# Performance work log

Measured on AMD Instinct MI355X. Metric: run time of the kernel, lower is better.

The kernel has to match this reference:

```python
import jax, jax.numpy as jnp
import numpy as np

FEATURE_HEIGHT = 50
FEATURE_WIDTH = 50


def setup_inputs() -> dict:
    key = jax.random.key(0)
    k1, k2, k3 = jax.random.split(key, 3)
    bs, K, H, D = 16, FEATURE_HEIGHT * FEATURE_WIDTH, 8, 32
    Q, L, P = 2000, 1, 4
    value = jax.random.normal(k1, (bs, K, H, D), dtype=jnp.float32)
    value_spatial_shapes = jnp.array([[FEATURE_HEIGHT, FEATURE_WIDTH]], dtype=jnp.int64)
    sampling_locations = jax.random.uniform(k2, (bs, Q, H, L, P, 2), dtype=jnp.float32)
    attention_weights = jax.random.uniform(k3, (bs, Q, H, L, P), dtype=jnp.float32)
    return {
        "value": value,
        "value_spatial_shapes": value_spatial_shapes,
        "sampling_locations": sampling_locations,
        "attention_weights": attention_weights,
    }


def _bilinear_sample(img, grid):
    """torch.F.grid_sample(mode='bilinear', padding_mode='zeros', align_corners=False).

    img:  (N, D, h, w)
    grid: (N, Q, P, 2), last dim (x, y) in [-1, 1]
    returns (N, D, Q, P)
    """
    N, D, h, w = img.shape
    # unnormalize (align_corners=False)
    x = (grid[..., 0] + 1.0) * (w * 0.5) - 0.5  # (N, Q, P)
    y = (grid[..., 1] + 1.0) * (h * 0.5) - 0.5
    x0 = jnp.floor(x)
    y0 = jnp.floor(y)
    x1 = x0 + 1.0
    y1 = y0 + 1.0
    wx1 = x - x0
    wx0 = 1.0 - wx1
    wy1 = y - y0
    wy0 = 1.0 - wy1

    img_flat = img.reshape(N, D, h * w)

    def corner(ix, iy, wgt):
        valid = ((ix >= 0) & (ix < w) & (iy >= 0) & (iy < h)).astype(img.dtype)
        ixc = jnp.clip(ix, 0, w - 1).astype(jnp.int32)
        iyc = jnp.clip(iy, 0, h - 1).astype(jnp.int32)
        idx = (iyc * w + ixc).reshape(N, -1)  # (N, Q*P)
        vals = jnp.take_along_axis(img_flat, idx[:, None, :], axis=2)  # (N, D, Q*P)
        vals = vals.reshape(N, D, *ix.shape[1:])  # (N, D, Q, P)
        return vals * (wgt * valid)[:, None]

    out = corner(x0, y0, wx0 * wy0)
    out = out + corner(x1, y0, wx1 * wy0)
    out = out + corner(x0, y1, wx0 * wy1)
    out = out + corner(x1, y1, wx1 * wy1)
    return out


def reference(value, value_spatial_shapes, sampling_locations, attention_weights):
    bs, K, H, D = value.shape
    _, Q, _, L, P, _ = sampling_locations.shape
    h, w = FEATURE_HEIGHT, FEATURE_WIDTH

    sampling_grids = 2.0 * sampling_locations - 1.0  # (bs, Q, H, L, P, 2)
    # value -> (bs*H, D, h, w)
    v = value.reshape(bs, K, H * D).transpose(0, 2, 1).reshape(bs * H, D, h, w)
    # level 0 grid -> (bs*H, Q, P, 2)
    g = jnp.transpose(sampling_grids[:, :, :, 0], (0, 2, 1, 3, 4)).reshape(bs * H, Q, P, 2)
    sampled = _bilinear_sample(v, g)  # (bs*H, D, Q, P)
    # attention weights -> (bs*H, 1, Q, L*P)
    aw = jnp.transpose(attention_weights, (0, 2, 1, 3, 4)).reshape(bs * H, 1, Q, L * P)
    out = (sampled * aw).sum(-1)  # (bs*H, D, Q)
    out = out.reshape(bs, H * D, Q).transpose(0, 2, 1)  # (bs, Q, H*D)
    return out
```

## Files before the change

kernel.cpp:

```cpp
#include <hip/hip_runtime.h>
#include <hip/hip_fp16.h>


#define FH 50
#define FW 50
#define KK (FH * FW)
#define NH 8
#define NQ 2000
#define NP 4
#define QHALF 1000

__global__ __launch_bounds__(512, 4) void deform_attn_kernel(
    const float* __restrict__ value,
    const float* __restrict__ loc,
    const float* __restrict__ attw,
    float* __restrict__ out)
{
    extern __shared__ ushort sv[];

    const int blk = blockIdx.x;
    const int xcd = blk & 7;
    const int s = blk >> 3;
    const int h = s & 7;
    const int chalf = (s >> 3) & 1;
    const int qh = (s >> 4) & 1;
    const int bph = (s >> 5) & 1;
    const int b = xcd + (bph << 3);

    {
        const float4* __restrict__ vsrc = (const float4*)value;
        const size_t vbase = (size_t)b * KK * 64 + h * 8 + chalf * 4;
        for (int i = threadIdx.x; i < KK * 4; i += 512) {
            const int k = i >> 2;
            const int cc = i & 3;
            const float4 f = vsrc[vbase + (size_t)k * 64 + cc];
            const __half2 p0 = __floats2half2_rn(f.x, f.y);
            const __half2 p1 = __floats2half2_rn(f.z, f.w);
            uint2 packed;
            packed.x = *(const unsigned int*)&p0;
            packed.y = *(const unsigned int*)&p1;
            *((uint2*)&sv[(size_t)i * 4]) = packed;
        }
    }
    __syncthreads();

    const int c = threadIdx.x & 3;
    const int grp = threadIdx.x >> 2;

    const float4* __restrict__ loc4 = (const float4*)loc;
    const float4* __restrict__ attw4 = (const float4*)attw;
    float4* __restrict__ out4 = (float4*)out;

    int qn = qh * QHALF + grp;
    int gidn = (b * NQ + qn) * NH + h;
    float4 l0 = loc4[(size_t)gidn * 2];
    float4 l1 = loc4[(size_t)gidn * 2 + 1];
    float4 a4 = attw4[gidn];
    int qcur = qn;

#pragma unroll 2
    for (int j = 0; j < 8; ++j) {
        const float4 c0 = l0, c1 = l1, ca = a4;
        const int q = qcur;
        if (j < 7) {
            const int qln = min((j + 1) * 128 + grp, QHALF - 1);
            qn = qh * QHALF + qln;
            gidn = (b * NQ + qn) * NH + h;
            l0 = loc4[(size_t)gidn * 2];
            l1 = loc4[(size_t)gidn * 2 + 1];
            a4 = attw4[gidn];
            qcur = qn;
        }

        const float pxx[NP] = {c0.x, c0.z, c1.x, c1.z};
        const float pyy[NP] = {c0.y, c0.w, c1.y, c1.w};
        const float awp[NP] = {ca.x, ca.y, ca.z, ca.w};

        int offs[16];
        float wts[16];
#pragma unroll
        for (int p = 0; p < NP; ++p) {
            const float fx = pxx[p] * (float)FW - 0.5f;
            const float fy = pyy[p] * (float)FH - 0.5f;
            const float x0f = floorf(fx);
            const float y0f = floorf(fy);
            const int x0 = (int)x0f, y0 = (int)y0f;
            const int x1 = x0 + 1, y1 = y0 + 1;
            const float wx1 = fx - x0f, wx0 = 1.f - wx1;
            const float wy1 = fy - y0f, wy0 = 1.f - wy1;

            const bool vx0 = (x0 >= 0) & (x0 < FW);
            const bool vx1 = (x1 >= 0) & (x1 < FW);
            const bool vy0 = (y0 >= 0) & (y0 < FH);
            const bool vy1 = (y1 >= 0) & (y1 < FH);

            const int cx0 = min(max(x0, 0), FW - 1);
            const int cx1 = min(max(x1, 0), FW - 1);
            const int cy0 = min(max(y0, 0), FH - 1);
            const int cy1 = min(max(y1, 0), FH - 1);

            offs[p * 4 + 0] = (cy0 * FW + cx0) * 16 + c * 4;
            offs[p * 4 + 1] = (cy0 * FW + cx1) * 16 + c * 4;
            offs[p * 4 + 2] = (cy1 * FW + cx0) * 16 + c * 4;
            offs[p * 4 + 3] = (cy1 * FW + cx1) * 16 + c * 4;

            wts[p * 4 + 0] = ((vx0 & vy0) ? (wx0 * wy0) : 0.f) * awp[p];
            wts[p * 4 + 1] = ((vx1 & vy0) ? (wx1 * wy0) : 0.f) * awp[p];
            wts[p * 4 + 2] = ((vx0 & vy1) ? (wx0 * wy1) : 0.f) * awp[p];
            wts[p * 4 + 3] = ((vx1 & vy1) ? (wx1 * wy1) : 0.f) * awp[p];
        }

        uint2 u[16];
#pragma unroll
        for (int i = 0; i < 16; ++i)
            u[i] = *((const uint2*)&sv[offs[i]]);

        float2 a01 = {0.f, 0.f}, a23 = {0.f, 0.f};
#pragma unroll
        for (int i = 0; i < 16; ++i) {
            const float w = wts[i];
            const float2 f0 = __half22float2(*(const __half2*)&u[i].x);
            const float2 f1 = __half22float2(*(const __half2*)&u[i].y);
            a01.x += w * f0.x; a01.y += w * f0.y;
            a23.x += w * f1.x; a23.y += w * f1.y;
        }

        out4[(size_t)(b * NQ + q) * 64 + h * 8 + chalf * 4 + c] =
            make_float4(a01.x, a01.y, a23.x, a23.y);
    }
}

extern "C" void kernel_launch(void* const* d_in, const int* in_sizes, int n_in,
                              void* d_out, int out_size, void* d_ws, size_t ws_size,
                              hipStream_t stream) {
    const float* value = (const float*)d_in[0];
    const float* loc  = (const float*)d_in[2];
    const float* attw = (const float*)d_in[3];
    float* out = (float*)d_out;

    hipFuncSetAttribute((const void*)deform_attn_kernel,
                        hipFuncAttributeMaxDynamicSharedMemorySize, 80000);

    deform_attn_kernel<<<512, 512, 80000, stream>>>(value, loc, attw, out);
}
```

Baseline: 119.6 us.

## Split channels between LDS-staged fp16 and direct global fp32 gathers

After: 141.6 us. +18.4%, slower.

```diff
diff --git a/kernel.cpp b/kernel.cpp
--- a/kernel.cpp
+++ b/kernel.cpp
@@ -8,7 +8,7 @@
 #define NH 8
 #define NQ 2000
 #define NP 4
-#define QHALF 1000
+#define QQ 500
 
 __global__ __launch_bounds__(512, 4) void deform_attn_kernel(
     const float* __restrict__ value,
@@ -22,25 +22,23 @@
     const int xcd = blk & 7;
     const int s = blk >> 3;
     const int h = s & 7;
-    const int chalf = (s >> 3) & 1;
-    const int qh = (s >> 4) & 1;
-    const int bph = (s >> 5) & 1;
+    const int qq = (s >> 3) & 3;
+    const int bph = s >> 5;
     const int b = xcd + (bph << 3);
 
-    {
-        const float4* __restrict__ vsrc = (const float4*)value;
-        const size_t vbase = (size_t)b * KK * 64 + h * 8 + chalf * 4;
-        for (int i = threadIdx.x; i < KK * 4; i += 512) {
-            const int k = i >> 2;
-            const int cc = i & 3;
-            const float4 f = vsrc[vbase + (size_t)k * 64 + cc];
-            const __half2 p0 = __floats2half2_rn(f.x, f.y);
-            const __half2 p1 = __floats2half2_rn(f.z, f.w);
-            uint2 packed;
-            packed.x = *(const unsigned int*)&p0;
-            packed.y = *(const unsigned int*)&p1;
-            *((uint2*)&sv[(size_t)i * 4]) = packed;
-        }
+    const float4* __restrict__ vsrc = (const float4*)value;
+    const size_t vrow = (size_t)b * KK * 64 + h * 8;
+
+    for (int i = threadIdx.x; i < KK * 4; i += 512) {
+        const int k = i >> 2;
+        const int cc = i & 3;
+        const float4 f = vsrc[vrow + (size_t)k * 64 + cc];
+        const __half2 p0 = __floats2half2_rn(f.x, f.y);
+        const __half2 p1 = __floats2half2_rn(f.z, f.w);
+        uint2 packed;
+        packed.x = *(const unsigned int*)&p0;
+        packed.y = *(const unsigned int*)&p1;
+        *((uint2*)&sv[(size_t)i * 4]) = packed;
     }
     __syncthreads();
 
@@ -50,25 +48,26 @@
     const float4* __restrict__ loc4 = (const float4*)loc;
     const float4* __restrict__ attw4 = (const float4*)attw;
     float4* __restrict__ out4 = (float4*)out;
+    const float4* __restrict__ gbase = vsrc + vrow + 4 + c;
 
-    int qn = qh * QHALF + grp;
-    int gidn = (b * NQ + qn) * NH + h;
-    float4 l0 = loc4[(size_t)gidn * 2];
-    float4 l1 = loc4[(size_t)gidn * 2 + 1];
-    float4 a4 = attw4[gidn];
-    int qcur = qn;
+    const int q0 = qq * QQ;
 
-#pragma unroll 2
-    for (int j = 0; j < 8; ++j) {
+    int q = q0 + grp;
+    int gid = (b * NQ + q) * NH + h;
+    float4 l0 = loc4[(size_t)gid * 2];
+    float4 l1 = loc4[(size_t)gid * 2 + 1];
+    float4 a4 = attw4[gid];
+    int qcur = q;
+
+    for (int j = 0; j < 4; ++j) {
         const float4 c0 = l0, c1 = l1, ca = a4;
-        const int q = qcur;
-        if (j < 7) {
-            const int qln = min((j + 1) * 128 + grp, QHALF - 1);
-            qn = qh * QHALF + qln;
-            gidn = (b * NQ + qn) * NH + h;
-            l0 = loc4[(size_t)gidn * 2];
-            l1 = loc4[(size_t)gidn * 2 + 1];
-            a4 = attw4[gidn];
+        const int qj = qcur;
+        if (j < 3) {
+            const int qn = q0 + min((j + 1) * 128 + grp, QQ - 1);
+            gid = (b * NQ + qn) * NH + h;
+            l0 = loc4[(size_t)gid * 2];
+            l1 = loc4[(size_t)gid * 2 + 1];
+            a4 = attw4[gid];
             qcur = qn;
         }
 
@@ -76,7 +75,7 @@
         const float pyy[NP] = {c0.y, c0.w, c1.y, c1.w};
         const float awp[NP] = {ca.x, ca.y, ca.z, ca.w};
 
-        int offs[16];
+        int krow[16];
         float wts[16];
 #pragma unroll
         for (int p = 0; p < NP; ++p) {
@@ -99,10 +98,10 @@
             const int cy0 = min(max(y0, 0), FH - 1);
             const int cy1 = min(max(y1, 0), FH - 1);
 
-            offs[p * 4 + 0] = (cy0 * FW + cx0) * 16 + c * 4;
-            offs[p * 4 + 1] = (cy0 * FW + cx1) * 16 + c * 4;
-            offs[p * 4 + 2] = (cy1 * FW + cx0) * 16 + c * 4;
-            offs[p * 4 + 3] = (cy1 * FW + cx1) * 16 + c * 4;
+            krow[p * 4 + 0] = cy0 * FW + cx0;
+            krow[p * 4 + 1] = cy0 * FW + cx1;
+            krow[p * 4 + 2] = cy1 * FW + cx0;
+            krow[p * 4 + 3] = cy1 * FW + cx1;
 
             wts[p * 4 + 0] = ((vx0 & vy0) ? (wx0 * wy0) : 0.f) * awp[p];
             wts[p * 4 + 1] = ((vx1 & vy0) ? (wx1 * wy0) : 0.f) * awp[p];
@@ -110,12 +109,18 @@
             wts[p * 4 + 3] = ((vx1 & vy1) ? (wx1 * wy1) : 0.f) * awp[p];
         }
 
+        float4 gv[16];
+#pragma unroll
+        for (int i = 0; i < 16; ++i)
+            gv[i] = gbase[(size_t)krow[i] * 64];
+
         uint2 u[16];
 #pragma unroll
         for (int i = 0; i < 16; ++i)
-            u[i] = *((const uint2*)&sv[offs[i]]);
+            u[i] = *((const uint2*)&sv[krow[i] * 16 + c * 4]);
 
         float2 a01 = {0.f, 0.f}, a23 = {0.f, 0.f};
+        float4 ahi = {0.f, 0.f, 0.f, 0.f};
 #pragma unroll
         for (int i = 0; i < 16; ++i) {
             const float w = wts[i];
@@ -123,10 +128,13 @@
             const float2 f1 = __half22float2(*(const __half2*)&u[i].y);
             a01.x += w * f0.x; a01.y += w * f0.y;
             a23.x += w * f1.x; a23.y += w * f1.y;
+            ahi.x += w * gv[i].x; ahi.y += w * gv[i].y;
+            ahi.z += w * gv[i].z; ahi.w += w * gv[i].w;
         }
 
-        out4[(size_t)(b * NQ + q) * 64 + h * 8 + chalf * 4 + c] =
-            make_float4(a01.x, a01.y, a23.x, a23.y);
+        const size_t obase = (size_t)(b * NQ + qj) * 64 + h * 8;
+        out4[obase + c] = make_float4(a01.x, a01.y, a23.x, a23.y);
+        out4[obase + 4 + c] = ahi;
     }
 }
 
```

## Pack horizontal pixel pairs in LDS and split channels four ways

Applied to the files above, without the earlier changes.

Result: slower. 129.0 us (+7.8%).

```diff
diff --git a/kernel.cpp b/kernel.cpp
--- a/kernel.cpp
+++ b/kernel.cpp
@@ -8,7 +8,6 @@
 #define NH 8
 #define NQ 2000
 #define NP 4
-#define QHALF 1000
 
 __global__ __launch_bounds__(512, 4) void deform_attn_kernel(
     const float* __restrict__ value,
@@ -22,53 +21,56 @@
     const int xcd = blk & 7;
     const int s = blk >> 3;
     const int h = s & 7;
-    const int chalf = (s >> 3) & 1;
-    const int qh = (s >> 4) & 1;
-    const int bph = (s >> 5) & 1;
+    const int cg = (s >> 3) & 3;
+    const int bph = s >> 5;
     const int b = xcd + (bph << 3);
 
+    const float4* __restrict__ value4 = (const float4*)value;
+
     {
-        const float4* __restrict__ vsrc = (const float4*)value;
-        const size_t vbase = (size_t)b * KK * 64 + h * 8 + chalf * 4;
-        for (int i = threadIdx.x; i < KK * 4; i += 512) {
-            const int k = i >> 2;
-            const int cc = i & 3;
-            const float4 f = vsrc[vbase + (size_t)k * 64 + cc];
-            const __half2 p0 = __floats2half2_rn(f.x, f.y);
-            const __half2 p1 = __floats2half2_rn(f.z, f.w);
-            uint2 packed;
-            packed.x = *(const unsigned int*)&p0;
-            packed.y = *(const unsigned int*)&p1;
-            *((uint2*)&sv[(size_t)i * 4]) = packed;
+        const size_t vq = ((size_t)b * KK * NH) * 8 + h * 8 + cg * 2;
+        for (int i = threadIdx.x; i < KK * 2; i += 512) {
+            const int k = i >> 1;
+            const int c = i & 1;
+            const int k2 = min(k + 1, KK - 1);
+            const float4 lo = value4[vq + (size_t)k * 64 + c];
+            const float4 hi = value4[vq + (size_t)k2 * 64 + c];
+            const __half2 p0 = __floats2half2_rn(lo.x, lo.y);
+            const __half2 p1 = __floats2half2_rn(lo.z, lo.w);
+            const __half2 p2 = __floats2half2_rn(hi.x, hi.y);
+            const __half2 p3 = __floats2half2_rn(hi.z, hi.w);
+            uint4 u;
+            u.x = *(const unsigned int*)&p0;
+            u.y = *(const unsigned int*)&p1;
+            u.z = *(const unsigned int*)&p2;
+            u.w = *(const unsigned int*)&p3;
+            *((uint4*)&sv[(size_t)i * 8]) = u;
         }
     }
     __syncthreads();
 
-    const int c = threadIdx.x & 3;
-    const int grp = threadIdx.x >> 2;
+    const int c = threadIdx.x & 1;
+    const int grp = threadIdx.x >> 1;
 
     const float4* __restrict__ loc4 = (const float4*)loc;
     const float4* __restrict__ attw4 = (const float4*)attw;
     float4* __restrict__ out4 = (float4*)out;
+    const size_t gbase = ((size_t)b * NQ) * NH + h;
 
-    int qn = qh * QHALF + grp;
-    int gidn = (b * NQ + qn) * NH + h;
-    float4 l0 = loc4[(size_t)gidn * 2];
-    float4 l1 = loc4[(size_t)gidn * 2 + 1];
-    float4 a4 = attw4[gidn];
-    int qcur = qn;
+    int q = grp;
+    float4 l0 = loc4[(gbase + (size_t)q * NH) * 2];
+    float4 l1 = loc4[(gbase + (size_t)q * NH) * 2 + 1];
+    float4 a4 = attw4[gbase + (size_t)q * NH];
+    int qcur = q;
 
-#pragma unroll 2
-    for (int j = 0; j < 8; ++j) {
+    for (int pass = 0; pass < 8; ++pass) {
         const float4 c0 = l0, c1 = l1, ca = a4;
-        const int q = qcur;
-        if (j < 7) {
-            const int qln = min((j + 1) * 128 + grp, QHALF - 1);
-            qn = qh * QHALF + qln;
-            gidn = (b * NQ + qn) * NH + h;
-            l0 = loc4[(size_t)gidn * 2];
-            l1 = loc4[(size_t)gidn * 2 + 1];
-            a4 = attw4[gidn];
+        const int qj = qcur;
+        if (pass < 7) {
+            const int qn = min((pass + 1) * 256 + grp, NQ - 1);
+            l0 = loc4[(gbase + (size_t)qn * NH) * 2];
+            l1 = loc4[(gbase + (size_t)qn * NH) * 2 + 1];
+            a4 = attw4[gbase + (size_t)qn * NH];
             qcur = qn;
         }
 
@@ -76,8 +78,7 @@
         const float pyy[NP] = {c0.y, c0.w, c1.y, c1.w};
         const float awp[NP] = {ca.x, ca.y, ca.z, ca.w};
 
-        int offs[16];
-        float wts[16];
+        float4 acc = {0.f, 0.f, 0.f, 0.f};
 #pragma unroll
         for (int p = 0; p < NP; ++p) {
             const float fx = pxx[p] * (float)FW - 0.5f;
@@ -85,48 +86,46 @@
             const float x0f = floorf(fx);
             const float y0f = floorf(fy);
             const int x0 = (int)x0f, y0 = (int)y0f;
-            const int x1 = x0 + 1, y1 = y0 + 1;
             const float wx1 = fx - x0f, wx0 = 1.f - wx1;
             const float wy1 = fy - y0f, wy0 = 1.f - wy1;
 
-            const bool vx0 = (x0 >= 0) & (x0 < FW);
-            const bool vx1 = (x1 >= 0) & (x1 < FW);
+            const int e = min(max(x0, 0), FW - 2);
+            const float wLo = (x0 == e) ? wx0 : ((x0 + 1 == e) ? wx1 : 0.f);
+            const float wHi = (x0 == e) ? wx1 : ((x0 == e + 1) ? wx0 : 0.f);
+
+            const int y1 = y0 + 1;
             const bool vy0 = (y0 >= 0) & (y0 < FH);
             const bool vy1 = (y1 >= 0) & (y1 < FH);
-
-            const int cx0 = min(max(x0, 0), FW - 1);
-            const int cx1 = min(max(x1, 0), FW - 1);
             const int cy0 = min(max(y0, 0), FH - 1);
             const int cy1 = min(max(y1, 0), FH - 1);
+            const float m0 = (vy0 ? wy0 : 0.f) * awp[p];
+            const float m1 = (vy1 ? wy1 : 0.f) * awp[p];
 
-            offs[p * 4 + 0] = (cy0 * FW + cx0) * 16 + c * 4;
-            offs[p * 4 + 1] = (cy0 * FW + cx1) * 16 + c * 4;
-            offs[p * 4 + 2] = (cy1 * FW + cx0) * 16 + c * 4;
-            offs[p * 4 + 3] = (cy1 * FW + cx1) * 16 + c * 4;
+            const int e0 = cy0 * FW + e;
+            const int e1 = cy1 * FW + e;
 
-            wts[p * 4 + 0] = ((vx0 & vy0) ? (wx0 * wy0) : 0.f) * awp[p];
-            wts[p * 4 + 1] = ((vx1 & vy0) ? (wx1 * wy0) : 0.f) * awp[p];
-            wts[p * 4 + 2] = ((vx0 & vy1) ? (wx0 * wy1) : 0.f) * awp[p];
-            wts[p * 4 + 3] = ((vx1 & vy1) ? (wx1 * wy1) : 0.f) * awp[p];
+            const uint4 u0 = *((const uint4*)&sv[e0 * 16 + c * 8]);
+            const uint4 u1 = *((const uint4*)&sv[e1 * 16 + c * 8]);
+
+            const float wA = m0 * wLo, wB = m0 * wHi;
+            const float wC = m1 * wLo, wD = m1 * wHi;
+
+            const float2 aL0 = __half22float2(*(const __half2*)&u0.x);
+            const float2 aL1 = __half22float2(*(const __half2*)&u0.y);
+            const float2 aH0 = __half22float2(*(const __half2*)&u0.z);
+            const float2 aH1 = __half22float2(*(const __half2*)&u0.w);
+            const float2 bL0 = __half22float2(*(const __half2*)&u1.x);
+            const float2 bL1 = __half22float2(*(const __half2*)&u1.y);
+            const float2 bH0 = __half22float2(*(const __half2*)&u1.z);
+            const float2 bH1 = __half22float2(*(const __half2*)&u1.w);
+
+            acc.x += wA * aL0.x + wB * aH0.x + wC * bL0.x + wD * bH0.x;
+            acc.y += wA * aL0.y + wB * aH0.y + wC * bL0.y + wD * bH0.y;
+            acc.z += wA * aL1.x + wB * aH1.x + wC * bL1.x + wD * bH1.x;
+            acc.w += wA * aL1.y + wB * aH1.y + wC * bL1.y + wD * bH1.y;
         }
 
-        uint2 u[16];
-#pragma unroll
-        for (int i = 0; i < 16; ++i)
-            u[i] = *((const uint2*)&sv[offs[i]]);
-
-        float2 a01 = {0.f, 0.f}, a23 = {0.f, 0.f};
-#pragma unroll
-        for (int i = 0; i < 16; ++i) {
-            const float w = wts[i];
-            const float2 f0 = __half22float2(*(const __half2*)&u[i].x);
-            const float2 f1 = __half22float2(*(const __half2*)&u[i].y);
-            a01.x += w * f0.x; a01.y += w * f0.y;
-            a23.x += w * f1.x; a23.y += w * f1.y;
-        }
-
-        out4[(size_t)(b * NQ + q) * 64 + h * 8 + chalf * 4 + c] =
-            make_float4(a01.x, a01.y, a23.x, a23.y);
+        out4[((size_t)b * NQ + qj) * 64 + h * 8 + cg * 2 + c] = acc;
     }
 }
 
```
